# Kernel optimization log

Measured on AMD Instinct MI355X. Metric: run time of the kernel, lower is better.

The kernel has to match this reference:

```python
import jax, jax.numpy as jnp
import numpy as np

QUERY_DIM = 512
KV_DIM = 64
N_AUX = 8
B = 65536
EPS = 1e-5


def setup_inputs() -> dict:
    key = jax.random.key(0)
    k1, k2, k3, k4, k5 = jax.random.split(key, 5)
    query = jax.random.normal(k1, (B, QUERY_DIM), dtype=jnp.float32)
    kv_stack = jax.random.normal(k2, (B, N_AUX, KV_DIM), dtype=jnp.float32)
    # Linear weights (torch nn.Linear stores W as [out, in]; y = x @ W.T)
    w_q = jax.random.normal(k3, (KV_DIM, QUERY_DIM), dtype=jnp.float32) / np.sqrt(QUERY_DIM)
    w_k = jax.random.normal(k4, (KV_DIM, KV_DIM), dtype=jnp.float32) / np.sqrt(KV_DIM)
    w_v = jax.random.normal(k5, (KV_DIM, KV_DIM), dtype=jnp.float32) / np.sqrt(KV_DIM)
    ln_gamma = jnp.ones((KV_DIM,), dtype=jnp.float32)
    ln_beta = jnp.zeros((KV_DIM,), dtype=jnp.float32)
    return {"query": query, "kv_stack": kv_stack, "w_q": w_q, "w_k": w_k,
            "w_v": w_v, "ln_gamma": ln_gamma, "ln_beta": ln_beta}


def reference(query, kv_stack, w_q, w_k, w_v, ln_gamma, ln_beta):
    scale = KV_DIM ** (-0.5)
    q = query @ w_q.T                                  # (B, kv_dim)
    k = jnp.einsum('bnd,ed->bne', kv_stack, w_k)       # (B, n_aux, kv_dim)
    v = jnp.einsum('bnd,ed->bne', kv_stack, w_v)       # (B, n_aux, kv_dim)
    scores = jnp.einsum('bd,bnd->bn', q, k) * scale    # (B, n_aux)
    attn_w = jax.nn.softmax(scores, axis=-1)
    out = jnp.einsum('bn,bnd->bd', attn_w, v)          # (B, kv_dim)
    # LayerNorm over last dim
    mu = jnp.mean(out, axis=-1, keepdims=True)
    var = jnp.var(out, axis=-1, keepdims=True)
    normed = (out - mu) / jnp.sqrt(var + EPS)
    return normed * ln_gamma + ln_beta
```

## Files before the change

### kernel.cpp

```cpp
#include <hip/hip_runtime.h>

#define QD 512
#define KD 64
#define NR 32
#define LDT 68
#define LDU 72

typedef __attribute__((ext_vector_type(8))) short short8;
typedef __attribute__((ext_vector_type(4))) float f32x4;

static __device__ __forceinline__ unsigned short f2bf(float f) {
  unsigned u = __builtin_bit_cast(unsigned, f);
  u += 0x7FFFu + ((u >> 16) & 1u);
  return (unsigned short)(u >> 16);
}
static __device__ __forceinline__ float bf2f(unsigned short s) {
  return __builtin_bit_cast(float, (unsigned)s << 16);
}
static __device__ __forceinline__ short8 pack8(f32x4 a, f32x4 b) {
  short8 r;
  r[0] = (short)f2bf(a[0]); r[1] = (short)f2bf(a[1]);
  r[2] = (short)f2bf(a[2]); r[3] = (short)f2bf(a[3]);
  r[4] = (short)f2bf(b[0]); r[5] = (short)f2bf(b[1]);
  r[6] = (short)f2bf(b[2]); r[7] = (short)f2bf(b[3]);
  return r;
}

static __device__ __forceinline__ void dma16(const void* g, void* l) {
  __builtin_amdgcn_global_load_lds(
      (const __attribute__((address_space(1))) void*)g,
      (__attribute__((address_space(3))) void*)l, 16, 0, 0);
}

__global__ __launch_bounds__(256) void prep_kernel(
    const float* __restrict__ w_q, const float* __restrict__ w_k,
    const float* __restrict__ w_v, unsigned short* __restrict__ mt,
    unsigned short* __restrict__ wvb) {
  const int tid = (int)(blockIdx.x * 256 + threadIdx.x);
  if (tid < QD * KD) {
    const int c = tid >> 9;
    const int d = tid & 511;
    float acc = 0.f;
#pragma unroll 8
    for (int e = 0; e < 64; ++e)
      acc = fmaf(w_q[e * QD + d], w_k[e * KD + c], acc);
    mt[c * QD + d] = f2bf(acc);
  } else {
    const int i = tid - QD * KD;
    if (i < KD * KD) wvb[i] = f2bf(w_v[i]);
  }
}

__global__ __launch_bounds__(256) void fused_kernel(
    const float* __restrict__ query,
    const float* __restrict__ kv,
    const unsigned short* __restrict__ mt,
    const unsigned short* __restrict__ wvb,
    const float* __restrict__ gamma,
    const float* __restrict__ beta,
    float* __restrict__ out) {
  __shared__ __align__(16) char regionA[NR * LDT * 4];
  __shared__ __align__(16) char regionB[8192];
  float* lds_t = (float*)regionA;
  unsigned short* lds_u = (unsigned short*)regionB;

  const int tid  = (int)threadIdx.x;
  const int w    = tid >> 6;
  const int l    = tid & 63;
  const int m    = l & 15;
  const int quad = l >> 4;
  const long row0 = (long)blockIdx.x * NR;

  const float* qsrc = query + (row0 + w * 8 + (l >> 3)) * QD
                            + (((l & 7) ^ ((l >> 3) & 7)) * 4);
  const unsigned short* msrc = mt + (w * 16 + (l >> 2)) * QD
                                  + (((l & 3) ^ ((l >> 4) & 3)) * 8);
  char* qdst = regionA + w * 1024;
  char* mdst = regionB + w * 1024;

  dma16(qsrc, qdst);            dma16(msrc, mdst);
  dma16(qsrc + 32, qdst + 4096); dma16(msrc + 32, mdst + 4096);

  const int a0off = m * 128 + (((2 * quad)     ^ (m & 7)) * 16);
  const int a1off = m * 128 + (((2 * quad + 1) ^ (m & 7)) * 16);
  const int boff  = (w * 16 + m) * 64 + ((quad ^ (m >> 2)) * 16);

  f32x4 acc[2];
  acc[0] = (f32x4){0.f, 0.f, 0.f, 0.f};
  acc[1] = (f32x4){0.f, 0.f, 0.f, 0.f};

#pragma unroll
  for (int c = 0; c < 16; ++c) {
    if (c < 15) { asm volatile("s_waitcnt vmcnt(2)" ::: "memory"); }
    else        { asm volatile("s_waitcnt vmcnt(0)" ::: "memory"); }
    __syncthreads();

    const char* qb = regionA + (c & 1) * 4096;
    const char* bbuf = regionB + (c & 1) * 4096;
    short8 bf = *(const short8*)(bbuf + boff);
#pragma unroll
    for (int rt = 0; rt < 2; ++rt) {
      f32x4 g0 = *(const f32x4*)(qb + rt * 2048 + a0off);
      f32x4 g1 = *(const f32x4*)(qb + rt * 2048 + a1off);
      short8 af = pack8(g0, g1);
      acc[rt] = __builtin_amdgcn_mfma_f32_16x16x32_bf16(af, bf, acc[rt], 0, 0, 0);
    }
    __syncthreads();
    if (c + 2 < 16) {
      dma16(qsrc + (c + 2) * 32, qdst + (c & 1) * 4096);
      dma16(msrc + (c + 2) * 32, mdst + (c & 1) * 4096);
    }
  }

#pragma unroll
  for (int rt = 0; rt < 2; ++rt)
#pragma unroll
    for (int r2 = 0; r2 < 4; ++r2)
      lds_t[(rt * 16 + quad * 4 + r2) * LDT + w * 16 + m] = acc[rt][r2];
  __syncthreads();

  const int rl = w * 8 + (l >> 3);
  const int o8 = l & 7;
  const int db = o8 * 8;
  const long brow = row0 + rl;

  const float* tp = lds_t + rl * LDT + db;
  f32x4 tv0 = ((const f32x4*)tp)[0];
  f32x4 tv1 = ((const f32x4*)tp)[1];

  float s[8];
  short8 kvb[8];
#pragma unroll
  for (int n = 0; n < 8; ++n) {
    const float* kp = kv + (brow * 8 + n) * 64 + db;
    f32x4 k0 = ((const f32x4*)kp)[0];
    f32x4 k1 = ((const f32x4*)kp)[1];
    f32x4 d = tv0 * k0 + tv1 * k1;
    s[n] = d[0] + d[1] + d[2] + d[3];
    kvb[n] = pack8(k0, k1);
  }
#pragma unroll
  for (int n = 0; n < 8; ++n) {
    s[n] += __shfl_xor(s[n], 1, 64);
    s[n] += __shfl_xor(s[n], 2, 64);
    s[n] += __shfl_xor(s[n], 4, 64);
  }
  float mx = s[0];
#pragma unroll
  for (int n = 1; n < 8; ++n) mx = fmaxf(mx, s[n]);
  float ev[8];
  float esum = 0.f;
#pragma unroll
  for (int n = 0; n < 8; ++n) { ev[n] = __expf((s[n] - mx) * 0.125f); esum += ev[n]; }
  const float rinv = 1.0f / esum;

  f32x4 u0 = {0.f, 0.f, 0.f, 0.f}, u1 = u0;
#pragma unroll
  for (int n = 0; n < 8; ++n) {
    const float a = ev[n];
    short8 p = kvb[n];
    u0 += a * (f32x4){bf2f((unsigned short)p[0]), bf2f((unsigned short)p[1]),
                      bf2f((unsigned short)p[2]), bf2f((unsigned short)p[3])};
    u1 += a * (f32x4){bf2f((unsigned short)p[4]), bf2f((unsigned short)p[5]),
                      bf2f((unsigned short)p[6]), bf2f((unsigned short)p[7])};
  }
  u0 *= rinv; u1 *= rinv;
  *(short8*)(lds_u + rl * LDU + db) = pack8(u0, u1);
  __syncthreads();

  short8 wvf0 = *(const short8*)(wvb + (w * 16 + m) * 64 + quad * 8);
  short8 wvf1 = *(const short8*)(wvb + (w * 16 + m) * 64 + 32 + quad * 8);
  f32x4 o[2];
  o[0] = (f32x4){0.f, 0.f, 0.f, 0.f};
  o[1] = (f32x4){0.f, 0.f, 0.f, 0.f};
#pragma unroll
  for (int rt = 0; rt < 2; ++rt) {
    short8 a0 = *(const short8*)(lds_u + (rt * 16 + m) * LDU + quad * 8);
    o[rt] = __builtin_amdgcn_mfma_f32_16x16x32_bf16(a0, wvf0, o[rt], 0, 0, 0);
    short8 a1 = *(const short8*)(lds_u + (rt * 16 + m) * LDU + 32 + quad * 8);
    o[rt] = __builtin_amdgcn_mfma_f32_16x16x32_bf16(a1, wvf1, o[rt], 0, 0, 0);
  }
#pragma unroll
  for (int rt = 0; rt < 2; ++rt)
#pragma unroll
    for (int r2 = 0; r2 < 4; ++r2)
      lds_t[(rt * 16 + quad * 4 + r2) * LDT + w * 16 + m] = o[rt][r2];
  __syncthreads();

  const float* op = lds_t + rl * LDT + db;
  f32x4 x0 = ((const f32x4*)op)[0];
  f32x4 x1 = ((const f32x4*)op)[1];
  f32x4 sv = x0 + x1;
  f32x4 sq = x0 * x0 + x1 * x1;
  float s1 = sv[0] + sv[1] + sv[2] + sv[3];
  float s2 = sq[0] + sq[1] + sq[2] + sq[3];
  s1 += __shfl_xor(s1, 1, 64); s1 += __shfl_xor(s1, 2, 64); s1 += __shfl_xor(s1, 4, 64);
  s2 += __shfl_xor(s2, 1, 64); s2 += __shfl_xor(s2, 2, 64); s2 += __shfl_xor(s2, 4, 64);
  const float mu   = s1 * 0.015625f;
  const float var  = s2 * 0.015625f - mu * mu;
  const float rstd = rsqrtf(var + 1e-5f);
  const float* gp = gamma + db;
  const float* bp = beta + db;
  float* dst = out + brow * 64 + db;
  {
    f32x4 g0 = ((const f32x4*)gp)[0], g1 = ((const f32x4*)gp)[1];
    f32x4 e0 = ((const f32x4*)bp)[0], e1 = ((const f32x4*)bp)[1];
    ((f32x4*)dst)[0] = (x0 - mu) * rstd * g0 + e0;
    ((f32x4*)dst)[1] = (x1 - mu) * rstd * g1 + e1;
  }
}

extern "C" void kernel_launch(void* const* d_in, const int* in_sizes, int n_in,
                              void* d_out, int out_size, void* d_ws, size_t ws_size,
                              hipStream_t stream) {
  const float* query = (const float*)d_in[0];
  const float* kv    = (const float*)d_in[1];
  const float* w_q   = (const float*)d_in[2];
  const float* w_k   = (const float*)d_in[3];
  const float* w_v   = (const float*)d_in[4];
  const float* gamma = (const float*)d_in[5];
  const float* beta  = (const float*)d_in[6];
  float* out = (float*)d_out;

  unsigned short* mt  = (unsigned short*)d_ws;
  unsigned short* wvb = mt + QD * KD;

  const int Bn = in_sizes[0] / QD;

  prep_kernel<<<(QD * KD + KD * KD + 255) / 256, 256, 0, stream>>>(w_q, w_k, w_v, mt, wvb);
  fused_kernel<<<Bn / NR, 256, 0, stream>>>(query, kv, mt, wvb, gamma, beta, out);
}
```

Before: 293.4 us.

## Split fused kernel into pipelined projection GEMM and separate attention kernel

The single fused kernel becomes two. The first is a query-projection GEMM with a 5-slot LDS ring and a prefetch depth of 4. It drops the second barrier and the XOR swizzle, and writes the projected q·M to the output buffer, used as scratch. The second kernel reads that scratch, issues all kv loads up front for more memory-level parallelism, and does the softmax, V projection and LayerNorm. This targets the latency-bound main loop, but adds a 16 MB intermediate round trip, an extra launch, and possible LDS bank conflicts from the unswizzled layout.

```diff
diff --git a/kernel.cpp b/kernel.cpp
--- a/kernel.cpp
+++ b/kernel.cpp
@@ -51,18 +51,12 @@
   }
 }
 
-__global__ __launch_bounds__(256) void fused_kernel(
+__global__ __launch_bounds__(256, 2) void gemm1_kernel(
     const float* __restrict__ query,
-    const float* __restrict__ kv,
     const unsigned short* __restrict__ mt,
-    const unsigned short* __restrict__ wvb,
-    const float* __restrict__ gamma,
-    const float* __restrict__ beta,
-    float* __restrict__ out) {
-  __shared__ __align__(16) char regionA[NR * LDT * 4];
-  __shared__ __align__(16) char regionB[8192];
-  float* lds_t = (float*)regionA;
-  unsigned short* lds_u = (unsigned short*)regionB;
+    float* __restrict__ tbuf) {
+  __shared__ __align__(16) char qring[5 * 4096];
+  __shared__ __align__(16) char mring[5 * 4096];
 
   const int tid  = (int)threadIdx.x;
   const int w    = tid >> 6;
@@ -71,19 +65,14 @@
   const int quad = l >> 4;
   const long row0 = (long)blockIdx.x * NR;
 
-  const float* qsrc = query + (row0 + w * 8 + (l >> 3)) * QD
-                            + (((l & 7) ^ ((l >> 3) & 7)) * 4);
-  const unsigned short* msrc = mt + (w * 16 + (l >> 2)) * QD
-                                  + (((l & 3) ^ ((l >> 4) & 3)) * 8);
-  char* qdst = regionA + w * 1024;
-  char* mdst = regionB + w * 1024;
-
-  dma16(qsrc, qdst);            dma16(msrc, mdst);
-  dma16(qsrc + 32, qdst + 4096); dma16(msrc + 32, mdst + 4096);
-
-  const int a0off = m * 128 + (((2 * quad)     ^ (m & 7)) * 16);
-  const int a1off = m * 128 + (((2 * quad + 1) ^ (m & 7)) * 16);
-  const int boff  = (w * 16 + m) * 64 + ((quad ^ (m >> 2)) * 16);
+  const float* qsrc = query + (row0 + (tid & 31)) * QD + ((tid >> 5) << 2);
+  const unsigned short* msrc = mt + (tid >> 2) * QD + ((tid & 3) << 3);
+
+#pragma unroll
+  for (int c = 0; c < 4; ++c) {
+    dma16(qsrc + c * 32, qring + c * 4096 + (w << 10));
+    dma16(msrc + c * 32, mring + c * 4096 + (w << 10));
+  }
 
   f32x4 acc[2];
   acc[0] = (f32x4){0.f, 0.f, 0.f, 0.f};
@@ -91,24 +80,25 @@
 
 #pragma unroll
   for (int c = 0; c < 16; ++c) {
-    if (c < 15) { asm volatile("s_waitcnt vmcnt(2)" ::: "memory"); }
-    else        { asm volatile("s_waitcnt vmcnt(0)" ::: "memory"); }
+    if (c <= 12)      { asm volatile("s_waitcnt vmcnt(6)" ::: "memory"); }
+    else if (c == 13) { asm volatile("s_waitcnt vmcnt(4)" ::: "memory"); }
+    else if (c == 14) { asm volatile("s_waitcnt vmcnt(2)" ::: "memory"); }
+    else              { asm volatile("s_waitcnt vmcnt(0)" ::: "memory"); }
     __syncthreads();
 
-    const char* qb = regionA + (c & 1) * 4096;
-    const char* bbuf = regionB + (c & 1) * 4096;
-    short8 bf = *(const short8*)(bbuf + boff);
+    const char* qb = qring + (c % 5) * 4096;
+    const char* bb = mring + (c % 5) * 4096;
+    short8 bf = *(const short8*)(bb + ((w * 16 + m) << 6) + (quad << 4));
 #pragma unroll
     for (int rt = 0; rt < 2; ++rt) {
-      f32x4 g0 = *(const f32x4*)(qb + rt * 2048 + a0off);
-      f32x4 g1 = *(const f32x4*)(qb + rt * 2048 + a1off);
-      short8 af = pack8(g0, g1);
-      acc[rt] = __builtin_amdgcn_mfma_f32_16x16x32_bf16(af, bf, acc[rt], 0, 0, 0);
+      f32x4 g0 = *(const f32x4*)(qb + (2 * quad) * 512 + ((rt * 16 + m) << 4));
+      f32x4 g1 = *(const f32x4*)(qb + (2 * quad + 1) * 512 + ((rt * 16 + m) << 4));
+      acc[rt] = __builtin_amdgcn_mfma_f32_16x16x32_bf16(pack8(g0, g1), bf,
+                                                        acc[rt], 0, 0, 0);
     }
-    __syncthreads();
-    if (c + 2 < 16) {
-      dma16(qsrc + (c + 2) * 32, qdst + (c & 1) * 4096);
-      dma16(msrc + (c + 2) * 32, mdst + (c & 1) * 4096);
+    if (c + 4 < 16) {
+      dma16(qsrc + (c + 4) * 32, qring + ((c + 4) % 5) * 4096 + (w << 10));
+      dma16(msrc + (c + 4) * 32, mring + ((c + 4) % 5) * 4096 + (w << 10));
     }
   }
 
@@ -116,28 +106,49 @@
   for (int rt = 0; rt < 2; ++rt)
 #pragma unroll
     for (int r2 = 0; r2 < 4; ++r2)
-      lds_t[(rt * 16 + quad * 4 + r2) * LDT + w * 16 + m] = acc[rt][r2];
-  __syncthreads();
+      tbuf[(row0 + rt * 16 + quad * 4 + r2) * 64 + w * 16 + m] = acc[rt][r2];
+}
+
+__global__ __launch_bounds__(256, 2) void attn_kernel(
+    const float* __restrict__ tbuf,
+    const float* __restrict__ kv,
+    const unsigned short* __restrict__ wvb,
+    const float* __restrict__ gamma,
+    const float* __restrict__ beta,
+    float* __restrict__ out) {
+  __shared__ __align__(16) float lds_t[NR * LDT];
+  __shared__ __align__(16) unsigned short lds_u[NR * LDU];
+
+  const int tid  = (int)threadIdx.x;
+  const int w    = tid >> 6;
+  const int l    = tid & 63;
+  const int m    = l & 15;
+  const int quad = l >> 4;
+  const long row0 = (long)blockIdx.x * NR;
 
   const int rl = w * 8 + (l >> 3);
   const int o8 = l & 7;
   const int db = o8 * 8;
   const long brow = row0 + rl;
 
-  const float* tp = lds_t + rl * LDT + db;
+  const float* tp = tbuf + brow * 64 + db;
   f32x4 tv0 = ((const f32x4*)tp)[0];
   f32x4 tv1 = ((const f32x4*)tp)[1];
+  const float* kp = kv + (brow * 8) * 64 + db;
+  f32x4 kf[16];
+#pragma unroll
+  for (int n = 0; n < 8; ++n) {
+    kf[2 * n]     = ((const f32x4*)(kp + n * 64))[0];
+    kf[2 * n + 1] = ((const f32x4*)(kp + n * 64))[1];
+  }
 
   float s[8];
-  short8 kvb[8];
-#pragma unroll
-  for (int n = 0; n < 8; ++n) {
-    const float* kp = kv + (brow * 8 + n) * 64 + db;
-    f32x4 k0 = ((const f32x4*)kp)[0];
-    f32x4 k1 = ((const f32x4*)kp)[1];
-    f32x4 d = tv0 * k0 + tv1 * k1;
+  short8 pk[8];
+#pragma unroll
+  for (int n = 0; n < 8; ++n) {
+    f32x4 d = tv0 * kf[2 * n] + tv1 * kf[2 * n + 1];
     s[n] = d[0] + d[1] + d[2] + d[3];
-    kvb[n] = pack8(k0, k1);
+    pk[n] = pack8(kf[2 * n], kf[2 * n + 1]);
   }
 #pragma unroll
   for (int n = 0; n < 8; ++n) {
@@ -158,7 +169,7 @@
 #pragma unroll
   for (int n = 0; n < 8; ++n) {
     const float a = ev[n];
-    short8 p = kvb[n];
+    short8 p = pk[n];
     u0 += a * (f32x4){bf2f((unsigned short)p[0]), bf2f((unsigned short)p[1]),
                       bf2f((unsigned short)p[2]), bf2f((unsigned short)p[3])};
     u1 += a * (f32x4){bf2f((unsigned short)p[4]), bf2f((unsigned short)p[5]),
@@ -199,15 +210,11 @@
   const float mu   = s1 * 0.015625f;
   const float var  = s2 * 0.015625f - mu * mu;
   const float rstd = rsqrtf(var + 1e-5f);
-  const float* gp = gamma + db;
-  const float* bp = beta + db;
+  f32x4 g0 = ((const f32x4*)(gamma + db))[0], g1 = ((const f32x4*)(gamma + db))[1];
+  f32x4 e0 = ((const f32x4*)(beta + db))[0],  e1 = ((const f32x4*)(beta + db))[1];
   float* dst = out + brow * 64 + db;
-  {
-    f32x4 g0 = ((const f32x4*)gp)[0], g1 = ((const f32x4*)gp)[1];
-    f32x4 e0 = ((const f32x4*)bp)[0], e1 = ((const f32x4*)bp)[1];
-    ((f32x4*)dst)[0] = (x0 - mu) * rstd * g0 + e0;
-    ((f32x4*)dst)[1] = (x1 - mu) * rstd * g1 + e1;
-  }
+  ((f32x4*)dst)[0] = (x0 - mu) * rstd * g0 + e0;
+  ((f32x4*)dst)[1] = (x1 - mu) * rstd * g1 + e1;
 }
 
 extern "C" void kernel_launch(void* const* d_in, const int* in_sizes, int n_in,
@@ -228,5 +235,6 @@
   const int Bn = in_sizes[0] / QD;
 
   prep_kernel<<<(QD * KD + KD * KD + 255) / 256, 256, 0, stream>>>(w_q, w_k, w_v, mt, wvb);
-  fused_kernel<<<Bn / NR, 256, 0, stream>>>(query, kv, mt, wvb, gamma, beta, out);
-}
+  gemm1_kernel<<<Bn / NR, 256, 0, stream>>>(query, mt, out);
+  attn_kernel<<<Bn / NR, 256, 0, stream>>>(out, kv, wvb, gamma, beta, out);
+}
```

New measurement: 300.2 us. 2.3% more time.
